# Performance work log

Measured on AMD Instinct MI355X. Metric: run time of the kernel, lower is better.

Reference implementation:

```python
import jax, jax.numpy as jnp
import numpy as np

B, D, E, H, OUT = 4096, 1024, 8, 4096, 1024


def setup_inputs() -> dict:
    key = jax.random.key(0)
    ks = jax.random.split(key, 8)
    s_in = 1.0 / np.sqrt(D)
    s_h = 1.0 / np.sqrt(H)
    return {
        "x": jax.random.normal(ks[0], (B, D), dtype=jnp.float32),
        "Wg": jax.random.uniform(ks[1], (D, E), minval=-s_in, maxval=s_in, dtype=jnp.float32),
        "bg": jnp.zeros((E,), dtype=jnp.float32),
        "W1": jax.random.uniform(ks[2], (E, D, H), minval=-s_in, maxval=s_in, dtype=jnp.float32),
        "b1": jnp.zeros((E, H), dtype=jnp.float32),
        "W2": jax.random.uniform(ks[3], (E, H, OUT), minval=-s_h, maxval=s_h, dtype=jnp.float32),
        "b2": jnp.zeros((E, OUT), dtype=jnp.float32),
        "w_bal": jnp.float32(0.01),
    }


def reference(x, Wg, bg, W1, b1, W2, b2, w_bal):
    # Gating: softmax then top-1 (== argmax of logits)
    gate_logits = x @ Wg + bg                      # [B, E]
    assign = jnp.argmax(gate_logits, axis=1)       # [B] top-1 expert
    onehot = jax.nn.one_hot(assign, E, dtype=x.dtype)  # [B, E] dispatch mask

    # Dense dispatch: run every expert MLP, combine by one-hot (top-1 select).
    # Original returns raw expert output (no gate-prob scaling).
    h = jax.nn.relu(jnp.einsum("bd,edh->ebh", x, W1) + b1[:, None, :])  # [E, B, H]
    y = jnp.einsum("ebh,eho->ebo", h, W2) + b2[:, None, :]              # [E, B, OUT]
    output = jnp.einsum("ebo,be->bo", y, onehot)                        # [B, OUT]

    # Load-balance loss on per-expert token counts
    loads = onehot.sum(axis=0)                     # [E]
    balance_loss = jnp.sum((loads - loads.mean()) ** 2) / E
    return output, balance_loss * w_bal
```

## Files before the change

kernel.cpp:

```cpp
#include <hip/hip_runtime.h>
#include <hip/hip_bf16.h>

typedef unsigned short u16;
typedef __attribute__((ext_vector_type(8))) short bf16x8;
typedef __attribute__((ext_vector_type(4))) float f32x4;

#define BTOK 4096
#define DDIM 1024
#define NEXP 8
#define HDIM 4096
#define ODIM 1024
#define MAXTILES 40
#define MAXROWS (MAXTILES * 128)

__device__ __forceinline__ u16 f2bf(float f) {
  unsigned u = __float_as_uint(f);
  return (u16)((u + 0x7FFFu + ((u >> 16) & 1u)) >> 16);
}

__device__ __forceinline__ void gload16(const void* g, void* l) {
  __builtin_amdgcn_global_load_lds(
      (const __attribute__((address_space(1))) void*)g,
      (__attribute__((address_space(3))) void*)l, 16, 0, 0);
}

__global__ __launch_bounds__(256) void gate_kernel(
    const float* __restrict__ x, const float* __restrict__ Wg,
    const float* __restrict__ bg, int* __restrict__ assign,
    int* __restrict__ counts) {
  int wave = threadIdx.x >> 6;
  int lane = threadIdx.x & 63;
  int b = blockIdx.x * 4 + wave;
  const float* xr = x + (size_t)b * DDIM;
  double acc[NEXP];
#pragma unroll
  for (int e = 0; e < NEXP; ++e) acc[e] = 0.0;
  for (int d = lane; d < DDIM; d += 64) {
    float xv = xr[d];
    const float4* wrow = (const float4*)(Wg + d * NEXP);
    float4 w0 = wrow[0], w1 = wrow[1];
    acc[0] += (double)xv * (double)w0.x;
    acc[1] += (double)xv * (double)w0.y;
    acc[2] += (double)xv * (double)w0.z;
    acc[3] += (double)xv * (double)w0.w;
    acc[4] += (double)xv * (double)w1.x;
    acc[5] += (double)xv * (double)w1.y;
    acc[6] += (double)xv * (double)w1.z;
    acc[7] += (double)xv * (double)w1.w;
  }
#pragma unroll
  for (int e = 0; e < NEXP; ++e) {
    double v = acc[e];
#pragma unroll
    for (int off = 32; off > 0; off >>= 1) v += __shfl_xor(v, off);
    acc[e] = v;
  }
  if (lane == 0) {
    int best = 0;
    double bv = acc[0] + (double)bg[0];
#pragma unroll
    for (int e = 1; e < NEXP; ++e) {
      double v = acc[e] + (double)bg[e];
      if (v > bv) { bv = v; best = e; }
    }
    assign[b] = best;
    atomicAdd(&counts[best], 1);
  }
}

__global__ void setup_kernel(const int* __restrict__ counts,
                             const float* __restrict__ wbal,
                             int* __restrict__ offp, int* __restrict__ tile_e,
                             int* __restrict__ tile_m, int* __restrict__ meta,
                             float* __restrict__ loss_out) {
  if (threadIdx.x != 0 || blockIdx.x != 0) return;
  int off = 0, nt = 0;
  for (int e = 0; e < NEXP; ++e) {
    offp[e] = off;
    int pc = (counts[e] + 127) & ~127;
    for (int t = 0; t < (pc >> 7); ++t) {
      tile_e[nt] = e;
      tile_m[nt] = off + t * 128;
      ++nt;
    }
    off += pc;
  }
  offp[NEXP] = off;
  meta[0] = nt;
  float mean = (float)BTOK / (float)NEXP;
  float s = 0.f;
  for (int e = 0; e < NEXP; ++e) {
    float d = (float)counts[e] - mean;
    s += d * d;
  }
  loss_out[0] = s / (float)NEXP * wbal[0];
}

__global__ __launch_bounds__(256) void gather_kernel(
    const float* __restrict__ x, const int* __restrict__ assign,
    const int* __restrict__ offp, int* __restrict__ fill,
    int* __restrict__ rowmap, u16* __restrict__ xg) {
  int b = blockIdx.x;
  __shared__ int srow;
  if (threadIdx.x == 0) {
    int e = assign[b];
    int pos = atomicAdd(&fill[e], 1);
    int row = offp[e] + pos;
    rowmap[row] = b;
    srow = row;
  }
  __syncthreads();
  int row = srow;
  float4 v = *(const float4*)(x + (size_t)b * DDIM + threadIdx.x * 4);
  ushort4 o;
  o.x = f2bf(v.x);
  o.y = f2bf(v.y);
  o.z = f2bf(v.z);
  o.w = f2bf(v.w);
  *(ushort4*)(xg + (size_t)row * DDIM + threadIdx.x * 4) = o;
}

__global__ __launch_bounds__(256) void transpose_conv(
    const float* __restrict__ W, u16* __restrict__ wt, int inN,
    size_t estrideIn, int k0, int n0, int KR, int NC) {
  const int e = blockIdx.z;
  const int kb = blockIdx.x * 64, nb = blockIdx.y * 64;
  __shared__ float lds[64][68];
  const float* src = W + (size_t)e * estrideIn + (size_t)k0 * inN + n0;
  const int t = threadIdx.x;
  const int rr = t >> 4, cc = (t & 15) * 4;
#pragma unroll
  for (int p = 0; p < 4; ++p) {
    float4 v = *(const float4*)(src + (size_t)(kb + rr + p * 16) * inN + nb + cc);
    *(float4*)&lds[rr + p * 16][cc] = v;
  }
  __syncthreads();
  const int n = t >> 2, kg = (t & 3) * 16;
  u16 tmp[16];
#pragma unroll
  for (int i = 0; i < 16; ++i) tmp[i] = f2bf(lds[kg + i][n]);
  u16* dst = wt + ((size_t)e * NC + nb + n) * KR + kb + kg;
  *(float4*)dst = *(float4*)&tmp[0];
  *(float4*)(dst + 8) = *(float4*)&tmp[8];
}

template <int K, int MODE>
__global__ __launch_bounds__(256) void moe_gemm(
    const u16* __restrict__ A, const u16* __restrict__ BT,
    const float* __restrict__ bias, const int* __restrict__ tile_e,
    const int* __restrict__ tile_m, const int* __restrict__ meta,
    const int* __restrict__ rowmap, u16* __restrict__ Hout,
    float* __restrict__ Cout, int NB, int ldh, int cOff, int biasLd) {
  if ((int)blockIdx.x >= meta[0]) return;
  const int e = tile_e[blockIdx.x];
  const int m0 = tile_m[blockIdx.x];
  const int n0 = blockIdx.y * 128;

  __shared__ __align__(16) u16 Alds[128 * 32];
  __shared__ __align__(16) u16 Blds[128 * 32];

  const int tid = threadIdx.x;
  const int lane = tid & 63;
  const int wave = tid >> 6;
  const int wr = wave >> 1, wc = wave & 1;
  const int fr = lane & 15;
  const int kqr = lane >> 4;

  const int u1 = tid + 256;
  const int rA0 = tid >> 2, kA0 = (tid & 3) ^ (rA0 & 3);
  const int rA1 = u1 >> 2, kA1 = (u1 & 3) ^ (rA1 & 3);
  const u16* aSrc0 = A + (size_t)(m0 + rA0) * K + kA0 * 8;
  const u16* aSrc1 = A + (size_t)(m0 + rA1) * K + kA1 * 8;
  const u16* bPan = BT + ((size_t)e * NB + n0) * K;
  const u16* bSrc0 = bPan + (size_t)rA0 * K + kA0 * 8;
  const u16* bSrc1 = bPan + (size_t)rA1 * K + kA1 * 8;
  u16* aDst0 = Alds + (size_t)(tid & ~63) * 8;
  u16* aDst1 = Alds + ((size_t)(tid & ~63) + 256) * 8;
  u16* bDst0 = Blds + (size_t)(tid & ~63) * 8;
  u16* bDst1 = Blds + ((size_t)(tid & ~63) + 256) * 8;

  int aOff[4], bOff[4];
#pragma unroll
  for (int i = 0; i < 4; ++i) {
    int r = wr * 64 + i * 16 + fr;
    aOff[i] = (r * 4 + (kqr ^ (r & 3))) * 8;
    int c = wc * 64 + i * 16 + fr;
    bOff[i] = (c * 4 + (kqr ^ (c & 3))) * 8;
  }

  f32x4 acc[4][4];
#pragma unroll
  for (int i = 0; i < 4; ++i)
#pragma unroll
    for (int j = 0; j < 4; ++j)
#pragma unroll
      for (int r = 0; r < 4; ++r) acc[i][j][r] = 0.f;

#pragma unroll 1
  for (int kt = 0; kt < K / 32; ++kt) {
    const int ko = kt * 32;
    gload16(aSrc0 + ko, aDst0);
    gload16(aSrc1 + ko, aDst1);
    gload16(bSrc0 + ko, bDst0);
    gload16(bSrc1 + ko, bDst1);
    __syncthreads();
    bf16x8 af[4], bfr[4];
#pragma unroll
    for (int i = 0; i < 4; ++i) {
      af[i] = *(const bf16x8*)&Alds[aOff[i]];
      bfr[i] = *(const bf16x8*)&Blds[bOff[i]];
    }
#pragma unroll
    for (int i = 0; i < 4; ++i)
#pragma unroll
      for (int j = 0; j < 4; ++j)
        acc[i][j] = __builtin_amdgcn_mfma_f32_16x16x32_bf16(af[i], bfr[j],
                                                            acc[i][j], 0, 0, 0);
    __syncthreads();
  }

  if constexpr (MODE == 0) {
#pragma unroll
    for (int i = 0; i < 4; ++i) {
      int rbase = m0 + wr * 64 + i * 16 + (lane >> 4) * 4;
#pragma unroll
      for (int j = 0; j < 4; ++j) {
        int col = n0 + wc * 64 + j * 16 + fr;
        float bv = bias[e * biasLd + cOff + col];
#pragma unroll
        for (int r = 0; r < 4; ++r) {
          float v = acc[i][j][r] + bv;
          v = v > 0.f ? v : 0.f;
          Hout[(size_t)(rbase + r) * ldh + col] = f2bf(v);
        }
      }
    }
  } else {
#pragma unroll
    for (int i = 0; i < 4; ++i) {
      int rbase = m0 + wr * 64 + i * 16 + (lane >> 4) * 4;
      int tok[4];
#pragma unroll
      for (int r = 0; r < 4; ++r) tok[r] = rowmap[rbase + r];
#pragma unroll
      for (int j = 0; j < 4; ++j) {
        int col = n0 + wc * 64 + j * 16 + fr;
        float bv = (MODE == 1) ? bias[e * biasLd + col] : 0.f;
#pragma unroll
        for (int r = 0; r < 4; ++r) {
          if (tok[r] >= 0) {
            size_t idx = (size_t)tok[r] * ODIM + col;
            if constexpr (MODE == 1)
              Cout[idx] = acc[i][j][r] + bv;
            else
              Cout[idx] += acc[i][j][r];
          }
        }
      }
    }
  }
}

template <int HC>
static void run_pipeline(const float* W1, const float* b1, const float* W2,
                         const float* b2, const u16* xg, u16* h, u16* wt,
                         const int* tile_e, const int* tile_m, const int* meta,
                         const int* rowmap, float* out, hipStream_t stream) {
  constexpr int NCH = HDIM / HC;
  for (int c = 0; c < NCH; ++c) {
    transpose_conv<<<dim3(DDIM / 64, HC / 64, NEXP), 256, 0, stream>>>(
        W1, wt, HDIM, (size_t)DDIM * HDIM, 0, c * HC, DDIM, HC);
    moe_gemm<DDIM, 0><<<dim3(MAXTILES, HC / 128), 256, 0, stream>>>(
        xg, wt, b1, tile_e, tile_m, meta, rowmap, h, nullptr, HC, HC, c * HC,
        HDIM);
    transpose_conv<<<dim3(HC / 64, ODIM / 64, NEXP), 256, 0, stream>>>(
        W2, wt, ODIM, (size_t)HDIM * ODIM, c * HC, 0, HC, ODIM);
    if (c == 0)
      moe_gemm<HC, 1><<<dim3(MAXTILES, ODIM / 128), 256, 0, stream>>>(
          h, wt, b2, tile_e, tile_m, meta, rowmap, nullptr, out, ODIM, 0, 0,
          ODIM);
    else
      moe_gemm<HC, 2><<<dim3(MAXTILES, ODIM / 128), 256, 0, stream>>>(
          h, wt, b2, tile_e, tile_m, meta, rowmap, nullptr, out, ODIM, 0, 0,
          ODIM);
  }
}

extern "C" void kernel_launch(void* const* d_in, const int* in_sizes, int n_in,
                              void* d_out, int out_size, void* d_ws,
                              size_t ws_size, hipStream_t stream) {
  const float* x = (const float*)d_in[0];
  const float* Wg = (const float*)d_in[1];
  const float* bg = (const float*)d_in[2];
  const float* W1 = (const float*)d_in[3];
  const float* b1 = (const float*)d_in[4];
  const float* W2 = (const float*)d_in[5];
  const float* b2 = (const float*)d_in[6];
  const float* wbal = (const float*)d_in[7];
  float* out = (float*)d_out;

  char* ws = (char*)d_ws;
  int* counts = (int*)(ws + 0);
  int* fill = (int*)(ws + 64);
  int* offp = (int*)(ws + 128);
  int* meta = (int*)(ws + 192);
  int* tile_e = (int*)(ws + 256);
  int* tile_m = (int*)(ws + 512);
  int* assign = (int*)(ws + 4096);
  int* rowmap = (int*)(ws + 4096 + BTOK * 4);
  u16* xg = (u16*)(ws + 65536);
  u16* h = (u16*)(ws + 65536 + (size_t)MAXROWS * DDIM * 2);

  const size_t base = 65536 + (size_t)MAXROWS * DDIM * 2;
  auto need = [&](int hc) {
    return base + (size_t)MAXROWS * hc * 2 + (size_t)NEXP * 1024 * hc * 2;
  };

  hipMemsetAsync(ws, 0, 4096, stream);
  hipMemsetAsync(rowmap, 0xFF, MAXROWS * 4, stream);
  hipMemsetAsync(xg, 0, (size_t)MAXROWS * DDIM * 2, stream);

  gate_kernel<<<BTOK / 4, 256, 0, stream>>>(x, Wg, bg, assign, counts);
  setup_kernel<<<1, 64, 0, stream>>>(counts, wbal, offp, tile_e, tile_m, meta,
                                     out + (size_t)BTOK * ODIM);
  gather_kernel<<<BTOK, 256, 0, stream>>>(x, assign, offp, fill, rowmap, xg);

  if (ws_size >= need(4096)) {
    u16* wt = (u16*)(ws + base + (size_t)MAXROWS * 4096 * 2);
    run_pipeline<4096>(W1, b1, W2, b2, xg, (u16*)(ws + base), wt, tile_e,
                       tile_m, meta, rowmap, out, stream);
  } else if (ws_size >= need(2048)) {
    u16* wt = (u16*)(ws + base + (size_t)MAXROWS * 2048 * 2);
    run_pipeline<2048>(W1, b1, W2, b2, xg, (u16*)(ws + base), wt, tile_e,
                       tile_m, meta, rowmap, out, stream);
  } else if (ws_size >= need(1024)) {
    u16* wt = (u16*)(ws + base + (size_t)MAXROWS * 1024 * 2);
    run_pipeline<1024>(W1, b1, W2, b2, xg, (u16*)(ws + base), wt, tile_e,
                       tile_m, meta, rowmap, out, stream);
  } else {
    u16* wt = (u16*)(ws + base + (size_t)MAXROWS * 512 * 2);
    run_pipeline<512>(W1, b1, W2, b2, xg, (u16*)(ws + base), wt, tile_e,
                      tile_m, meta, rowmap, out, stream);
  }
}
```

Measured before the change: 367.4 us.

## Double-buffer GEMM LDS, split-K second GEMM with bf16 partials and reduce kernel

The GEMM main loop now double-buffers its LDS tiles so global loads for the next K step overlap the MFMAs on the current one, and it uses a different swizzle. Workgroup IDs are remapped across the grid. The second GEMM is split along K into two z-slices that write bf16 partial buffers, and a new reduce kernel adds the partials and the bias and scatters rows to tokens. The chunk size is fixed at 2048 with hardcoded workspace offsets, which drops the fallback for smaller workspaces. Accumulating partials in bf16 also costs accuracy.

```diff
diff --git a/kernel.cpp b/kernel.cpp
--- a/kernel.cpp
+++ b/kernel.cpp
@@ -3,6 +3,7 @@
 
 typedef unsigned short u16;
 typedef __attribute__((ext_vector_type(8))) short bf16x8;
+typedef __attribute__((ext_vector_type(8))) unsigned short u16x8;
 typedef __attribute__((ext_vector_type(4))) float f32x4;
 
 #define BTOK 4096
@@ -10,12 +11,16 @@
 #define NEXP 8
 #define HDIM 4096
 #define ODIM 1024
+#define HC 2048
 #define MAXTILES 40
 #define MAXROWS (MAXTILES * 128)
 
 __device__ __forceinline__ u16 f2bf(float f) {
   unsigned u = __float_as_uint(f);
   return (u16)((u + 0x7FFFu + ((u >> 16) & 1u)) >> 16);
+}
+__device__ __forceinline__ float bf2f(u16 v) {
+  return __uint_as_float(((unsigned)v) << 16);
 }
 
 __device__ __forceinline__ void gload16(const void* g, void* l) {
@@ -144,20 +149,26 @@
   *(float4*)(dst + 8) = *(float4*)&tmp[8];
 }
 
-template <int K, int MODE>
+template <int MODE>
 __global__ __launch_bounds__(256) void moe_gemm(
-    const u16* __restrict__ A, const u16* __restrict__ BT,
-    const float* __restrict__ bias, const int* __restrict__ tile_e,
-    const int* __restrict__ tile_m, const int* __restrict__ meta,
-    const int* __restrict__ rowmap, u16* __restrict__ Hout,
-    float* __restrict__ Cout, int NB, int ldh, int cOff, int biasLd) {
-  if ((int)blockIdx.x >= meta[0]) return;
-  const int e = tile_e[blockIdx.x];
-  const int m0 = tile_m[blockIdx.x];
-  const int n0 = blockIdx.y * 128;
-
-  __shared__ __align__(16) u16 Alds[128 * 32];
-  __shared__ __align__(16) u16 Blds[128 * 32];
+    const u16* __restrict__ A, int lda, const u16* __restrict__ BT, int ldb,
+    int nbRows, const float* __restrict__ bias, int biasLd, int cOff,
+    const int* __restrict__ tile_e, const int* __restrict__ tile_m,
+    const int* __restrict__ meta, u16* __restrict__ Hout, int ldh,
+    u16* __restrict__ P, size_t pStride) {
+  const int nx = gridDim.x;
+  const int nwg = nx * gridDim.y;
+  const int orig = blockIdx.y * nx + blockIdx.x;
+  const int q = nwg >> 3;
+  const int wg = (orig & 7) * q + (orig >> 3);
+  const int bx = wg % nx, by = wg / nx;
+  if (bx >= meta[0]) return;
+  const int e = tile_e[bx];
+  const int m0 = tile_m[bx];
+  const int n0 = by * 128;
+  const int kOff = blockIdx.z << 10;
+
+  __shared__ __align__(16) u16 lds[2 * 8192];
 
   const int tid = threadIdx.x;
   const int lane = tid & 63;
@@ -166,26 +177,23 @@
   const int fr = lane & 15;
   const int kqr = lane >> 4;
 
-  const int u1 = tid + 256;
-  const int rA0 = tid >> 2, kA0 = (tid & 3) ^ (rA0 & 3);
-  const int rA1 = u1 >> 2, kA1 = (u1 & 3) ^ (rA1 & 3);
-  const u16* aSrc0 = A + (size_t)(m0 + rA0) * K + kA0 * 8;
-  const u16* aSrc1 = A + (size_t)(m0 + rA1) * K + kA1 * 8;
-  const u16* bPan = BT + ((size_t)e * NB + n0) * K;
-  const u16* bSrc0 = bPan + (size_t)rA0 * K + kA0 * 8;
-  const u16* bSrc1 = bPan + (size_t)rA1 * K + kA1 * 8;
-  u16* aDst0 = Alds + (size_t)(tid & ~63) * 8;
-  u16* aDst1 = Alds + ((size_t)(tid & ~63) + 256) * 8;
-  u16* bDst0 = Blds + (size_t)(tid & ~63) * 8;
-  u16* bDst1 = Blds + ((size_t)(tid & ~63) + 256) * 8;
+  const int r0 = tid >> 2, k0 = (tid & 3) ^ ((r0 >> 1) & 3);
+  const int r1 = (tid + 256) >> 2, k1 = ((tid + 256) & 3) ^ ((r1 >> 1) & 3);
+  const u16* aS0 = A + (size_t)(m0 + r0) * lda + kOff + k0 * 8;
+  const u16* aS1 = A + (size_t)(m0 + r1) * lda + kOff + k1 * 8;
+  const u16* bPan = BT + ((size_t)e * nbRows + n0) * ldb + kOff;
+  const u16* bS0 = bPan + (size_t)r0 * ldb + k0 * 8;
+  const u16* bS1 = bPan + (size_t)r1 * ldb + k1 * 8;
+  const int dst0 = (tid & ~63) * 8;
+  const int dst1 = dst0 + 2048;
 
   int aOff[4], bOff[4];
 #pragma unroll
   for (int i = 0; i < 4; ++i) {
     int r = wr * 64 + i * 16 + fr;
-    aOff[i] = (r * 4 + (kqr ^ (r & 3))) * 8;
+    aOff[i] = (r * 4 + (kqr ^ ((r >> 1) & 3))) * 8;
     int c = wc * 64 + i * 16 + fr;
-    bOff[i] = (c * 4 + (kqr ^ (c & 3))) * 8;
+    bOff[i] = (c * 4 + (kqr ^ ((c >> 1) & 3))) * 8;
   }
 
   f32x4 acc[4][4];
@@ -196,19 +204,21 @@
 #pragma unroll
       for (int r = 0; r < 4; ++r) acc[i][j][r] = 0.f;
 
-#pragma unroll 1
-  for (int kt = 0; kt < K / 32; ++kt) {
+  auto stage = [&](int c, int kt) {
     const int ko = kt * 32;
-    gload16(aSrc0 + ko, aDst0);
-    gload16(aSrc1 + ko, aDst1);
-    gload16(bSrc0 + ko, bDst0);
-    gload16(bSrc1 + ko, bDst1);
-    __syncthreads();
+    u16* base = lds + c * 8192;
+    gload16(aS0 + ko, base + dst0);
+    gload16(aS1 + ko, base + dst1);
+    gload16(bS0 + ko, base + 4096 + dst0);
+    gload16(bS1 + ko, base + 4096 + dst1);
+  };
+  auto compute = [&](int c) {
+    const u16* base = lds + c * 8192;
     bf16x8 af[4], bfr[4];
 #pragma unroll
     for (int i = 0; i < 4; ++i) {
-      af[i] = *(const bf16x8*)&Alds[aOff[i]];
-      bfr[i] = *(const bf16x8*)&Blds[bOff[i]];
+      af[i] = *(const bf16x8*)(base + aOff[i]);
+      bfr[i] = *(const bf16x8*)(base + 4096 + bOff[i]);
     }
 #pragma unroll
     for (int i = 0; i < 4; ++i)
@@ -216,8 +226,19 @@
       for (int j = 0; j < 4; ++j)
         acc[i][j] = __builtin_amdgcn_mfma_f32_16x16x32_bf16(af[i], bfr[j],
                                                             acc[i][j], 0, 0, 0);
+  };
+
+  stage(0, 0);
+  __syncthreads();
+  int cur = 0;
+#pragma unroll 1
+  for (int kt = 0; kt < 31; ++kt) {
+    stage(cur ^ 1, kt + 1);
+    compute(cur);
     __syncthreads();
-  }
+    cur ^= 1;
+  }
+  compute(cur);
 
   if constexpr (MODE == 0) {
 #pragma unroll
@@ -236,53 +257,56 @@
       }
     }
   } else {
+    u16* Pp = P + blockIdx.z * pStride;
 #pragma unroll
     for (int i = 0; i < 4; ++i) {
       int rbase = m0 + wr * 64 + i * 16 + (lane >> 4) * 4;
-      int tok[4];
-#pragma unroll
-      for (int r = 0; r < 4; ++r) tok[r] = rowmap[rbase + r];
 #pragma unroll
       for (int j = 0; j < 4; ++j) {
         int col = n0 + wc * 64 + j * 16 + fr;
-        float bv = (MODE == 1) ? bias[e * biasLd + col] : 0.f;
 #pragma unroll
         for (int r = 0; r < 4; ++r) {
-          if (tok[r] >= 0) {
-            size_t idx = (size_t)tok[r] * ODIM + col;
-            if constexpr (MODE == 1)
-              Cout[idx] = acc[i][j][r] + bv;
-            else
-              Cout[idx] += acc[i][j][r];
-          }
+          size_t idx = (size_t)(rbase + r) * ODIM + col;
+          if constexpr (MODE == 1)
+            Pp[idx] = f2bf(acc[i][j][r]);
+          else
+            Pp[idx] = f2bf(bf2f(Pp[idx]) + acc[i][j][r]);
         }
       }
     }
   }
 }
 
-template <int HC>
-static void run_pipeline(const float* W1, const float* b1, const float* W2,
-                         const float* b2, const u16* xg, u16* h, u16* wt,
-                         const int* tile_e, const int* tile_m, const int* meta,
-                         const int* rowmap, float* out, hipStream_t stream) {
-  constexpr int NCH = HDIM / HC;
-  for (int c = 0; c < NCH; ++c) {
-    transpose_conv<<<dim3(DDIM / 64, HC / 64, NEXP), 256, 0, stream>>>(
-        W1, wt, HDIM, (size_t)DDIM * HDIM, 0, c * HC, DDIM, HC);
-    moe_gemm<DDIM, 0><<<dim3(MAXTILES, HC / 128), 256, 0, stream>>>(
-        xg, wt, b1, tile_e, tile_m, meta, rowmap, h, nullptr, HC, HC, c * HC,
-        HDIM);
-    transpose_conv<<<dim3(HC / 64, ODIM / 64, NEXP), 256, 0, stream>>>(
-        W2, wt, ODIM, (size_t)HDIM * ODIM, c * HC, 0, HC, ODIM);
-    if (c == 0)
-      moe_gemm<HC, 1><<<dim3(MAXTILES, ODIM / 128), 256, 0, stream>>>(
-          h, wt, b2, tile_e, tile_m, meta, rowmap, nullptr, out, ODIM, 0, 0,
-          ODIM);
-    else
-      moe_gemm<HC, 2><<<dim3(MAXTILES, ODIM / 128), 256, 0, stream>>>(
-          h, wt, b2, tile_e, tile_m, meta, rowmap, nullptr, out, ODIM, 0, 0,
-          ODIM);
+__global__ __launch_bounds__(256) void reduce_kernel(
+    const u16* __restrict__ P, size_t pStride, const int* __restrict__ rowmap,
+    const int* __restrict__ tile_e, const int* __restrict__ tile_m,
+    const int* __restrict__ meta, const float* __restrict__ b2,
+    float* __restrict__ out) {
+  if ((int)blockIdx.x >= meta[0]) return;
+  const int e = tile_e[blockIdx.x];
+  const int row = tile_m[blockIdx.x] + (threadIdx.x >> 1);
+  const int tok = rowmap[row];
+  if (tok < 0) return;
+  const int c0 = blockIdx.y * 128 + (threadIdx.x & 1) * 64;
+  const u16* p0 = P + (size_t)row * ODIM;
+  const u16* p1 = p0 + pStride;
+  float* o = out + (size_t)tok * ODIM;
+#pragma unroll
+  for (int j = 0; j < 8; ++j) {
+    int c = c0 + j * 8;
+    u16x8 a = *(const u16x8*)(p0 + c);
+    u16x8 b = *(const u16x8*)(p1 + c);
+    float4 v0, v1;
+    v0.x = bf2f(a[0]) + bf2f(b[0]) + b2[e * ODIM + c + 0];
+    v0.y = bf2f(a[1]) + bf2f(b[1]) + b2[e * ODIM + c + 1];
+    v0.z = bf2f(a[2]) + bf2f(b[2]) + b2[e * ODIM + c + 2];
+    v0.w = bf2f(a[3]) + bf2f(b[3]) + b2[e * ODIM + c + 3];
+    v1.x = bf2f(a[4]) + bf2f(b[4]) + b2[e * ODIM + c + 4];
+    v1.y = bf2f(a[5]) + bf2f(b[5]) + b2[e * ODIM + c + 5];
+    v1.z = bf2f(a[6]) + bf2f(b[6]) + b2[e * ODIM + c + 6];
+    v1.w = bf2f(a[7]) + bf2f(b[7]) + b2[e * ODIM + c + 7];
+    *(float4*)(o + c) = v0;
+    *(float4*)(o + c + 4) = v1;
   }
 }
 
@@ -307,14 +331,13 @@
   int* tile_e = (int*)(ws + 256);
   int* tile_m = (int*)(ws + 512);
   int* assign = (int*)(ws + 4096);
-  int* rowmap = (int*)(ws + 4096 + BTOK * 4);
+  int* rowmap = (int*)(ws + 20480);
   u16* xg = (u16*)(ws + 65536);
-  u16* h = (u16*)(ws + 65536 + (size_t)MAXROWS * DDIM * 2);
-
-  const size_t base = 65536 + (size_t)MAXROWS * DDIM * 2;
-  auto need = [&](int hc) {
-    return base + (size_t)MAXROWS * hc * 2 + (size_t)NEXP * 1024 * hc * 2;
-  };
+  u16* h = (u16*)(ws + 10551296);
+  u16* wt = (u16*)(ws + 52494336);
+  u16* P = (u16*)(ws + 86048768);
+  const size_t hChunk = (size_t)MAXROWS * HC;
+  const size_t pStride = (size_t)MAXROWS * ODIM;
 
   hipMemsetAsync(ws, 0, 4096, stream);
   hipMemsetAsync(rowmap, 0xFF, MAXROWS * 4, stream);
@@ -325,21 +348,24 @@
                                      out + (size_t)BTOK * ODIM);
   gather_kernel<<<BTOK, 256, 0, stream>>>(x, assign, offp, fill, rowmap, xg);
 
-  if (ws_size >= need(4096)) {
-    u16* wt = (u16*)(ws + base + (size_t)MAXROWS * 4096 * 2);
-    run_pipeline<4096>(W1, b1, W2, b2, xg, (u16*)(ws + base), wt, tile_e,
-                       tile_m, meta, rowmap, out, stream);
-  } else if (ws_size >= need(2048)) {
-    u16* wt = (u16*)(ws + base + (size_t)MAXROWS * 2048 * 2);
-    run_pipeline<2048>(W1, b1, W2, b2, xg, (u16*)(ws + base), wt, tile_e,
-                       tile_m, meta, rowmap, out, stream);
-  } else if (ws_size >= need(1024)) {
-    u16* wt = (u16*)(ws + base + (size_t)MAXROWS * 1024 * 2);
-    run_pipeline<1024>(W1, b1, W2, b2, xg, (u16*)(ws + base), wt, tile_e,
-                       tile_m, meta, rowmap, out, stream);
-  } else {
-    u16* wt = (u16*)(ws + base + (size_t)MAXROWS * 512 * 2);
-    run_pipeline<512>(W1, b1, W2, b2, xg, (u16*)(ws + base), wt, tile_e,
-                      tile_m, meta, rowmap, out, stream);
-  }
-}
+  for (int c = 0; c < 2; ++c) {
+    u16* hc = h + (size_t)c * hChunk;
+    transpose_conv<<<dim3(DDIM / 64, HC / 64, NEXP), 256, 0, stream>>>(
+        W1, wt, HDIM, (size_t)DDIM * HDIM, 0, c * HC, DDIM, HC);
+    moe_gemm<0><<<dim3(MAXTILES, HC / 128, 1), 256, 0, stream>>>(
+        xg, DDIM, wt, DDIM, HC, b1, HDIM, c * HC, tile_e, tile_m, meta, hc, HC,
+        nullptr, 0);
+    transpose_conv<<<dim3(HC / 64, ODIM / 64, NEXP), 256, 0, stream>>>(
+        W2, wt, ODIM, (size_t)HDIM * ODIM, c * HC, 0, HC, ODIM);
+    if (c == 0)
+      moe_gemm<1><<<dim3(MAXTILES, ODIM / 128, 2), 256, 0, stream>>>(
+          hc, HC, wt, HC, ODIM, nullptr, 0, 0, tile_e, tile_m, meta, nullptr, 0,
+          P, pStride);
+    else
+      moe_gemm<2><<<dim3(MAXTILES, ODIM / 128, 2), 256, 0, stream>>>(
+          hc, HC, wt, HC, ODIM, nullptr, 0, 0, tile_e, tile_m, meta, nullptr, 0,
+          P, pStride);
+  }
+  reduce_kernel<<<dim3(MAXTILES, ODIM / 128), 256, 0, stream>>>(
+      P, pStride, rowmap, tile_e, tile_m, meta, b2, out);
+}
```

Result: no change. 370.1 us (+0.7%).
